# Kernel optimization log

Measured on AMD Instinct MI355X. Metric: run time of the kernel, lower is better.

## Reference

```python
import jax, jax.numpy as jnp
import numpy as np

EPS = 1e-12  # tf.contrib layer_norm default epsilon
FORGET_BIAS = 1.0  # tf LSTMCell default


def _layer_norm(x, gamma, beta):
    mu = jnp.mean(x, axis=-1, keepdims=True)
    var = jnp.mean(jnp.square(x - mu), axis=-1, keepdims=True)
    return (x - mu) * jax.lax.rsqrt(var + EPS) * gamma + beta


def setup_inputs() -> dict:
    key = jax.random.key(0)
    ks = jax.random.split(key, 16)
    B, T, OBS, ACT, H = 256, 512, 256, 64, 64
    N = B * T
    s = 0.05
    inp = {
        "obs": jax.random.normal(ks[0], (N, OBS), jnp.float32),
        "action": jax.random.normal(ks[1], (N, ACT), jnp.float32),
        "c0": jnp.zeros((B, H), jnp.float32),
        "h0": jnp.zeros((B, H), jnp.float32),
        "W_obs": jax.random.normal(ks[2], (OBS, H), jnp.float32) * s,
        "b_obs": jnp.zeros((H,), jnp.float32),
        "g1": jnp.ones((H,), jnp.float32),
        "beta1": jnp.zeros((H,), jnp.float32),
        "W_act": jax.random.normal(ks[3], (ACT, H), jnp.float32) * s,
        "b_act": jnp.zeros((H,), jnp.float32),
        "g2": jnp.ones((H,), jnp.float32),
        "beta2": jnp.zeros((H,), jnp.float32),
        "W_lstm": jax.random.normal(ks[4], (2 * H + H, 4 * H), jnp.float32) * s,
        "b_lstm": jnp.zeros((4 * H,), jnp.float32),
        "g3": jnp.ones((H,), jnp.float32),
        "beta3": jnp.zeros((H,), jnp.float32),
        "W_out": jax.random.uniform(ks[5], (H, 1), jnp.float32, -0.003, 0.003),
        "b_out": jnp.zeros((1,), jnp.float32),
        "batch_size": B,
        "step_size": T,
    }
    return inp


def reference(obs, action, c0, h0, W_obs, b_obs, g1, beta1, W_act, b_act, g2, beta2,
              W_lstm, b_lstm, g3, beta3, W_out, b_out, batch_size, step_size):
    H = 64
    # obs branch (output is overwritten below — faithful to source bug)
    x = jnp.maximum(_layer_norm(obs @ W_obs + b_obs, g1, beta1), 0.0)
    # action branch
    yd = action @ W_act + b_act
    x = _layer_norm(yd, g2, beta2)  # BUG in source: overwrites obs branch
    y = jnp.maximum(yd, 0.0)
    xy = jnp.concatenate([x, y], axis=-1)  # [B*T, 128]
    rnn_in = xy.reshape(batch_size, step_size, 2 * H).transpose(1, 0, 2)  # [T,B,128]

    def step(carry, x_t):
        c, h = carry
        z = jnp.concatenate([x_t, h], axis=-1) @ W_lstm + b_lstm  # [B,4H]
        i, j, f, o = jnp.split(z, 4, axis=-1)  # tf LSTMCell gate order
        c_new = c * jax.nn.sigmoid(f + FORGET_BIAS) + jax.nn.sigmoid(i) * jnp.tanh(j)
        h_new = jax.nn.sigmoid(o) * jnp.tanh(c_new)
        return (c_new, h_new), h_new

    (c_fin, h_fin), hs = jax.lax.scan(step, (c0, h0), rnn_in)  # hs: [T,B,H]
    out = hs.transpose(1, 0, 2).reshape(batch_size * step_size, H)
    out = _layer_norm(out, g3, beta3)
    q = out @ W_out + b_out  # [B*T, 1]
    return q, c_fin, h_fin
```

## Files before the change

kernel.cpp:

```cpp
#include <hip/hip_runtime.h>

#define HD 64
#define TT 512
#define BB 256
#define NROWS (BB * TT)

typedef _Float16 half2_t __attribute__((ext_vector_type(2)));

__device__ __forceinline__ float rl(float v, int k) {
  return __uint_as_float(__builtin_amdgcn_readlane(__float_as_uint(v), k));
}
__device__ __forceinline__ float wsum(float v) {
#pragma unroll
  for (int m = 32; m >= 1; m >>= 1) v += __shfl_xor(v, m, 64);
  return v;
}
__device__ __forceinline__ float sigmoidf_(float x) {
  return 1.0f / (1.0f + __expf(-x));
}
__device__ __forceinline__ float tanhf_(float x) {
  return 1.0f - 2.0f / (__expf(2.0f * x) + 1.0f);
}
__device__ __forceinline__ unsigned short f2bf(float f) {
  unsigned int u = __float_as_uint(f);
  u = (u + 0x7fffu + ((u >> 16) & 1u)) >> 16;
  return (unsigned short)u;
}
__device__ __forceinline__ float ldz(const float* p) { return *p; }
__device__ __forceinline__ float ldz(const unsigned short* p) {
  return __uint_as_float(((unsigned int)(*p)) << 16);
}
__device__ __forceinline__ void store8(float* p, float4 a, float4 b) {
  *(float4*)p = a;
  *(float4*)(p + 4) = b;
}
__device__ __forceinline__ void store8(unsigned short* p, float4 a, float4 b) {
  union { unsigned short us[8]; int4 v; } u;
  u.us[0] = f2bf(a.x); u.us[1] = f2bf(a.y); u.us[2] = f2bf(a.z); u.us[3] = f2bf(a.w);
  u.us[4] = f2bf(b.x); u.us[5] = f2bf(b.y); u.us[6] = f2bf(b.z); u.us[7] = f2bf(b.w);
  *(int4*)p = u.v;
}
__device__ __forceinline__ float4 fma4(float4 a, float s, float4 w) {
  a.x += s * w.x; a.y += s * w.y; a.z += s * w.z; a.w += s * w.w;
  return a;
}
__device__ __forceinline__ float4 add4(float4 a, float4 b) {
  a.x += b.x; a.y += b.y; a.z += b.z; a.w += b.w;
  return a;
}

__device__ __forceinline__ float dot2(half2_t a, half2_t b, float acc) {
#if __has_builtin(__builtin_amdgcn_fdot2)
  return __builtin_amdgcn_fdot2(a, b, acc, false);
#else
  return acc + (float)a.x * (float)b.x + (float)a.y * (float)b.y;
#endif
}

__device__ __forceinline__ half2_t pkrtz(float a, float b) {
  return __builtin_bit_cast(half2_t, __builtin_amdgcn_cvt_pkrtz(a, b));
}

template <typename ZT>
__global__ __launch_bounds__(256) void kA(const float* __restrict__ act,
                                          const float* __restrict__ Wact,
                                          const float* __restrict__ bact,
                                          const float* __restrict__ g2,
                                          const float* __restrict__ beta2,
                                          const float* __restrict__ Wl,
                                          const float* __restrict__ bl,
                                          ZT* __restrict__ Zx) {
  __shared__ float xy[64][128];
  const int tid = threadIdx.x;
  const int lane = tid & 63;
  const int wv = tid >> 6;
  const int r0blk = blockIdx.x * 64;

  float wreg[64];
#pragma unroll
  for (int k = 0; k < 64; ++k) wreg[k] = Wact[k * 64 + lane];
  const float ba = bact[lane], gg = g2[lane], bb = beta2[lane];

  for (int i = 0; i < 16; ++i) {
    const int r = i * 4 + wv;
    const int row = r0blk + r;
    const float a = act[row * 64 + lane];
    float yd = ba;
#pragma unroll
    for (int k = 0; k < 64; ++k) yd += rl(a, k) * wreg[k];
    const float mu = wsum(yd) * (1.0f / 64.0f);
    const float d = yd - mu;
    const float var = wsum(d * d) * (1.0f / 64.0f);
    const float x = d * rsqrtf(var + 1e-12f) * gg + bb;
    xy[r][lane] = x;
    xy[r][64 + lane] = fmaxf(yd, 0.0f);
  }
  __syncthreads();

  const int tc = tid & 31;
  const int tr = tid >> 5;
  const int c0 = tc * 8;
  float4 accA[8], accB[8];
#pragma unroll
  for (int r = 0; r < 8; ++r) {
    accA[r] = make_float4(0.f, 0.f, 0.f, 0.f);
    accB[r] = make_float4(0.f, 0.f, 0.f, 0.f);
  }
  for (int kk = 0; kk < 128; kk += 4) {
    float4 xv[8];
#pragma unroll
    for (int r = 0; r < 8; ++r) xv[r] = *(const float4*)&xy[tr * 8 + r][kk];
#pragma unroll
    for (int dk = 0; dk < 4; ++dk) {
      const float4 wa = *(const float4*)&Wl[(kk + dk) * 256 + c0];
      const float4 wb = *(const float4*)&Wl[(kk + dk) * 256 + c0 + 4];
#pragma unroll
      for (int r = 0; r < 8; ++r) {
        const float xr = (dk == 0) ? xv[r].x : (dk == 1) ? xv[r].y : (dk == 2) ? xv[r].z : xv[r].w;
        accA[r] = fma4(accA[r], xr, wa);
        accB[r] = fma4(accB[r], xr, wb);
      }
    }
  }
  const float4 bla = *(const float4*)&bl[c0];
  const float4 blb = *(const float4*)&bl[c0 + 4];
#pragma unroll
  for (int r = 0; r < 8; ++r) {
    const int row = r0blk + tr * 8 + r;
    store8(&Zx[(size_t)row * 256 + c0], add4(accA[r], bla), add4(accB[r], blb));
  }
}

template <typename ZT>
__global__ __launch_bounds__(64, 1) void kB4(const ZT* __restrict__ Zx,
                                             const float* __restrict__ Wl,
                                             const float* __restrict__ c0p,
                                             const float* __restrict__ h0p,
                                             float* __restrict__ hs,
                                             float* __restrict__ cfin,
                                             float* __restrict__ hfin) {
  const int l = threadIdx.x;
  const int b = blockIdx.x;

  half2_t wi[32], wj[32], wf[32], wo[32];
#pragma unroll
  for (int p = 0; p < 32; ++p) {
    const float* r0 = &Wl[(128 + p) * 256];
    const float* r1 = &Wl[(128 + p + 32) * 256];
    wi[p] = pkrtz(r0[l], r1[l]);
    wj[p] = pkrtz(r0[64 + l], r1[64 + l]);
    wf[p] = pkrtz(r0[128 + l], r1[128 + l]);
    wo[p] = pkrtz(r0[192 + l], r1[192 + l]);
  }

  float c = c0p[b * 64 + l];
  float h = h0p[b * 64 + l];

  const ZT* zrow = Zx + (size_t)b * TT * 256;
  float* hsrow = hs + (size_t)b * TT * 64;

#define LD4(PI, PJ, PF, PO, T)                       \
  PI = ldz(&zrow[(size_t)(T) * 256 + 0 + l]);        \
  PJ = ldz(&zrow[(size_t)(T) * 256 + 64 + l]);       \
  PF = ldz(&zrow[(size_t)(T) * 256 + 128 + l]);      \
  PO = ldz(&zrow[(size_t)(T) * 256 + 192 + l]);

  float pAi, pAj, pAf, pAo, pBi, pBj, pBf, pBo;
  float pCi, pCj, pCf, pCo, pDi, pDj, pDf, pDo;
  LD4(pAi, pAj, pAf, pAo, 0)
  LD4(pBi, pBj, pBf, pBo, 1)
  LD4(pCi, pCj, pCf, pCo, 2)
  LD4(pDi, pDj, pDf, pDo, 3)

#define STEP(PI, PJ, PF, PO, T)                                               \
  {                                                                           \
    const float hx = __shfl_xor(h, 32, 64);                                   \
    const half2_t hp = pkrtz(h, hx);                                          \
    const unsigned int hpu = __builtin_bit_cast(unsigned int, hp);            \
    float zi = PI, zj = PJ, zf = PF, zo = PO;                                 \
    _Pragma("unroll") for (int p = 0; p < 32; ++p) {                          \
      const unsigned int hu = __builtin_amdgcn_readlane(hpu, p);              \
      const half2_t hb = __builtin_bit_cast(half2_t, hu);                     \
      zi = dot2(hb, wi[p], zi);                                               \
      zj = dot2(hb, wj[p], zj);                                               \
      zf = dot2(hb, wf[p], zf);                                               \
      zo = dot2(hb, wo[p], zo);                                               \
    }                                                                         \
    int tn = (T) + 4;                                                         \
    if (tn > TT - 1) tn = TT - 1;                                             \
    LD4(PI, PJ, PF, PO, tn)                                                   \
    c = c * sigmoidf_(zf + 1.0f) + sigmoidf_(zi) * tanhf_(zj);                \
    h = sigmoidf_(zo) * tanhf_(c);                                            \
    hsrow[(size_t)(T) * 64 + l] = h;                                          \
  }

#pragma unroll 1
  for (int t = 0; t < TT; t += 4) {
    STEP(pAi, pAj, pAf, pAo, t)
    STEP(pBi, pBj, pBf, pBo, t + 1)
    STEP(pCi, pCj, pCf, pCo, t + 2)
    STEP(pDi, pDj, pDf, pDo, t + 3)
  }
#undef STEP
#undef LD4

  cfin[b * 64 + l] = c;
  hfin[b * 64 + l] = h;
}

__global__ __launch_bounds__(256) void kC(const float* __restrict__ hs,
                                          const float* __restrict__ g3,
                                          const float* __restrict__ beta3,
                                          const float* __restrict__ Wout,
                                          const float* __restrict__ bout,
                                          float* __restrict__ q) {
  const int lane = threadIdx.x & 63;
  const int wv = threadIdx.x >> 6;
  const float g = g3[lane], be = beta3[lane], wo = Wout[lane], bo = bout[0];
  for (int n = blockIdx.x * 4 + wv; n < NROWS; n += gridDim.x * 4) {
    const float v = hs[(size_t)n * 64 + lane];
    const float mu = wsum(v) * (1.0f / 64.0f);
    const float d = v - mu;
    const float var = wsum(d * d) * (1.0f / 64.0f);
    const float xn = d * rsqrtf(var + 1e-12f) * g + be;
    const float s = wsum(xn * wo);
    if (lane == 0) q[n] = s + bo;
  }
}

extern "C" void kernel_launch(void* const* d_in, const int* in_sizes, int n_in,
                              void* d_out, int out_size, void* d_ws, size_t ws_size,
                              hipStream_t stream) {
  const float* action = (const float*)d_in[1];
  const float* c0 = (const float*)d_in[2];
  const float* h0 = (const float*)d_in[3];
  const float* Wact = (const float*)d_in[8];
  const float* bact = (const float*)d_in[9];
  const float* g2 = (const float*)d_in[10];
  const float* b2 = (const float*)d_in[11];
  const float* Wl = (const float*)d_in[12];
  const float* bl = (const float*)d_in[13];
  const float* g3 = (const float*)d_in[14];
  const float* b3 = (const float*)d_in[15];
  const float* Wout = (const float*)d_in[16];
  const float* bout = (const float*)d_in[17];

  float* q = (float*)d_out;
  float* cfin = q + NROWS;
  float* hfin = cfin + BB * HD;

  const size_t zx32 = (size_t)NROWS * 256 * sizeof(float);
  const size_t zx16 = (size_t)NROWS * 256 * sizeof(unsigned short);
  const size_t hsb = (size_t)NROWS * 64 * sizeof(float);

  if (ws_size >= zx32 + hsb) {
    float* Zx = (float*)d_ws;
    float* hs = (float*)((char*)d_ws + zx32);
    kA<float><<<NROWS / 64, 256, 0, stream>>>(action, Wact, bact, g2, b2, Wl, bl, Zx);
    kB4<float><<<BB, 64, 0, stream>>>(Zx, Wl, c0, h0, hs, cfin, hfin);
    kC<<<2048, 256, 0, stream>>>(hs, g3, b3, Wout, bout, q);
  } else {
    unsigned short* Zx = (unsigned short*)d_ws;
    float* hs = (float*)((char*)d_ws + zx16);
    kA<unsigned short><<<NROWS / 64, 256, 0, stream>>>(action, Wact, bact, g2, b2, Wl, bl, Zx);
    kB4<unsigned short><<<BB, 64, 0, stream>>>(Zx, Wl, c0, h0, hs, cfin, hfin);
    kC<<<2048, 256, 0, stream>>>(hs, g3, b3, Wout, bout, q);
  }
}
```

Before: 484.1 us.

## Split LSTM recurrent matvec across four waves with LDS partial-sum reduction

The recurrent kernel now uses 256 threads per batch row instead of 64. Each wave holds a 16-row slice of the hidden weights and computes partial gate sums, which are exchanged through a double-buffered LDS array after a barrier. This shortens the serial chain of dot products per timestep. In exchange it adds a workgroup barrier and LDS round trip every step, and every wave redundantly computes the activations.

```diff
diff --git a/kernel.cpp b/kernel.cpp
--- a/kernel.cpp
+++ b/kernel.cpp
@@ -6,6 +6,7 @@
 #define NROWS (BB * TT)
 
 typedef _Float16 half2_t __attribute__((ext_vector_type(2)));
+typedef __attribute__((ext_vector_type(4))) float f32x4;
 
 __device__ __forceinline__ float rl(float v, int k) {
   return __uint_as_float(__builtin_amdgcn_readlane(__float_as_uint(v), k));
@@ -48,7 +49,6 @@
   a.x += b.x; a.y += b.y; a.z += b.z; a.w += b.w;
   return a;
 }
-
 __device__ __forceinline__ float dot2(half2_t a, half2_t b, float acc) {
 #if __has_builtin(__builtin_amdgcn_fdot2)
   return __builtin_amdgcn_fdot2(a, b, acc, false);
@@ -56,7 +56,6 @@
   return acc + (float)a.x * (float)b.x + (float)a.y * (float)b.y;
 #endif
 }
-
 __device__ __forceinline__ half2_t pkrtz(float a, float b) {
   return __builtin_bit_cast(half2_t, __builtin_amdgcn_cvt_pkrtz(a, b));
 }
@@ -132,26 +131,27 @@
 }
 
 template <typename ZT>
-__global__ __launch_bounds__(64, 1) void kB4(const ZT* __restrict__ Zx,
-                                             const float* __restrict__ Wl,
-                                             const float* __restrict__ c0p,
-                                             const float* __restrict__ h0p,
-                                             float* __restrict__ hs,
-                                             float* __restrict__ cfin,
-                                             float* __restrict__ hfin) {
-  const int l = threadIdx.x;
+__global__ __launch_bounds__(256, 1) void kB8(const ZT* __restrict__ Zx,
+                                              const float* __restrict__ Wl,
+                                              const float* __restrict__ c0p,
+                                              const float* __restrict__ h0p,
+                                              float* __restrict__ hs,
+                                              float* __restrict__ cfin,
+                                              float* __restrict__ hfin) {
+  __shared__ float part[2][4][4][64];
+  const int tid = threadIdx.x;
+  const int w = tid >> 6;
+  const int l = tid & 63;
   const int b = blockIdx.x;
-
-  half2_t wi[32], wj[32], wf[32], wo[32];
-#pragma unroll
-  for (int p = 0; p < 32; ++p) {
-    const float* r0 = &Wl[(128 + p) * 256];
-    const float* r1 = &Wl[(128 + p + 32) * 256];
-    wi[p] = pkrtz(r0[l], r1[l]);
-    wj[p] = pkrtz(r0[64 + l], r1[64 + l]);
-    wf[p] = pkrtz(r0[128 + l], r1[128 + l]);
-    wo[p] = pkrtz(r0[192 + l], r1[192 + l]);
-  }
+  const int k0 = w * 16;
+
+  half2_t wp[4][8];
+#pragma unroll
+  for (int g = 0; g < 4; ++g)
+#pragma unroll
+    for (int p = 0; p < 8; ++p)
+      wp[g][p] = pkrtz(Wl[(128 + k0 + p) * 256 + g * 64 + l],
+                       Wl[(128 + k0 + p + 8) * 256 + g * 64 + l]);
 
   float c = c0p[b * 64 + l];
   float h = h0p[b * 64 + l];
@@ -172,26 +172,39 @@
   LD4(pCi, pCj, pCf, pCo, 2)
   LD4(pDi, pDj, pDf, pDo, 3)
 
-#define STEP(PI, PJ, PF, PO, T)                                               \
-  {                                                                           \
-    const float hx = __shfl_xor(h, 32, 64);                                   \
-    const half2_t hp = pkrtz(h, hx);                                          \
-    const unsigned int hpu = __builtin_bit_cast(unsigned int, hp);            \
-    float zi = PI, zj = PJ, zf = PF, zo = PO;                                 \
-    _Pragma("unroll") for (int p = 0; p < 32; ++p) {                          \
-      const unsigned int hu = __builtin_amdgcn_readlane(hpu, p);              \
-      const half2_t hb = __builtin_bit_cast(half2_t, hu);                     \
-      zi = dot2(hb, wi[p], zi);                                               \
-      zj = dot2(hb, wj[p], zj);                                               \
-      zf = dot2(hb, wf[p], zf);                                               \
-      zo = dot2(hb, wo[p], zo);                                               \
-    }                                                                         \
-    int tn = (T) + 4;                                                         \
-    if (tn > TT - 1) tn = TT - 1;                                             \
-    LD4(PI, PJ, PF, PO, tn)                                                   \
-    c = c * sigmoidf_(zf + 1.0f) + sigmoidf_(zi) * tanhf_(zj);                \
-    h = sigmoidf_(zo) * tanhf_(c);                                            \
-    hsrow[(size_t)(T) * 64 + l] = h;                                          \
+#define STEP(PI, PJ, PF, PO, T)                                                \
+  {                                                                            \
+    const float hx = __shfl_xor(h, 8, 64);                                     \
+    const half2_t hp = pkrtz(h, hx);                                           \
+    const unsigned int hpu = __builtin_bit_cast(unsigned int, hp);             \
+    float s0 = 0.f, s1 = 0.f, s2 = 0.f, s3 = 0.f;                              \
+    _Pragma("unroll") for (int p = 0; p < 8; ++p) {                            \
+      const unsigned int hu = __builtin_amdgcn_readlane(hpu, k0 + p);          \
+      const half2_t hb = __builtin_bit_cast(half2_t, hu);                      \
+      s0 = dot2(hb, wp[0][p], s0);                                             \
+      s1 = dot2(hb, wp[1][p], s1);                                             \
+      s2 = dot2(hb, wp[2][p], s2);                                             \
+      s3 = dot2(hb, wp[3][p], s3);                                             \
+    }                                                                          \
+    part[(T) & 1][w][0][l] = s0;                                               \
+    part[(T) & 1][w][1][l] = s1;                                               \
+    part[(T) & 1][w][2][l] = s2;                                               \
+    part[(T) & 1][w][3][l] = s3;                                               \
+    asm volatile("s_waitcnt lgkmcnt(0)\n\ts_barrier" ::: "memory");            \
+    const float zi = PI + part[(T) & 1][0][0][l] + part[(T) & 1][1][0][l] +    \
+                     part[(T) & 1][2][0][l] + part[(T) & 1][3][0][l];          \
+    const float zj = PJ + part[(T) & 1][0][1][l] + part[(T) & 1][1][1][l] +    \
+                     part[(T) & 1][2][1][l] + part[(T) & 1][3][1][l];          \
+    const float zf = PF + part[(T) & 1][0][2][l] + part[(T) & 1][1][2][l] +    \
+                     part[(T) & 1][2][2][l] + part[(T) & 1][3][2][l];          \
+    const float zo = PO + part[(T) & 1][0][3][l] + part[(T) & 1][1][3][l] +    \
+                     part[(T) & 1][2][3][l] + part[(T) & 1][3][3][l];          \
+    int tn = (T) + 4;                                                          \
+    if (tn > TT - 1) tn = TT - 1;                                              \
+    LD4(PI, PJ, PF, PO, tn)                                                    \
+    c = c * sigmoidf_(zf + 1.0f) + sigmoidf_(zi) * tanhf_(zj);                 \
+    h = sigmoidf_(zo) * tanhf_(c);                                             \
+    if (w == 0) hsrow[(size_t)(T) * 64 + l] = h;                               \
   }
 
 #pragma unroll 1
@@ -204,8 +217,10 @@
 #undef STEP
 #undef LD4
 
-  cfin[b * 64 + l] = c;
-  hfin[b * 64 + l] = h;
+  if (w == 0) {
+    cfin[b * 64 + l] = c;
+    hfin[b * 64 + l] = h;
+  }
 }
 
 __global__ __launch_bounds__(256) void kC(const float* __restrict__ hs,
@@ -257,13 +272,13 @@
     float* Zx = (float*)d_ws;
     float* hs = (float*)((char*)d_ws + zx32);
     kA<float><<<NROWS / 64, 256, 0, stream>>>(action, Wact, bact, g2, b2, Wl, bl, Zx);
-    kB4<float><<<BB, 64, 0, stream>>>(Zx, Wl, c0, h0, hs, cfin, hfin);
+    kB8<float><<<BB, 256, 0, stream>>>(Zx, Wl, c0, h0, hs, cfin, hfin);
     kC<<<2048, 256, 0, stream>>>(hs, g3, b3, Wout, bout, q);
   } else {
     unsigned short* Zx = (unsigned short*)d_ws;
     float* hs = (float*)((char*)d_ws + zx16);
     kA<unsigned short><<<NROWS / 64, 256, 0, stream>>>(action, Wact, bact, g2, b2, Wl, bl, Zx);
-    kB4<unsigned short><<<BB, 64, 0, stream>>>(Zx, Wl, c0, h0, hs, cfin, hfin);
+    kB8<unsigned short><<<BB, 256, 0, stream>>>(Zx, Wl, c0, h0, hs, cfin, hfin);
     kC<<<2048, 256, 0, stream>>>(hs, g3, b3, Wout, bout, q);
   }
 }
```

Result: faster. 464.1 us (-4.1%).
